# Kernel optimization log

Measured on AMD Instinct MI355X. Metric: run time of the kernel, lower is better.

Reference implementation:

```python
import math
import jax, jax.numpy as jnp
import numpy as np

H = 8
C_HIDDEN = 32
C_Q = 256


def setup_inputs() -> dict:
    key = jax.random.key(0)
    ks = jax.random.split(key, 9)
    B, S, Q, K = 1, 128, 256, 256
    q_x = jax.random.normal(ks[0], (B, S, Q, C_Q), dtype=jnp.float32)
    kv_x = jax.random.normal(ks[1], (B, S, K, C_Q), dtype=jnp.float32)
    bias1 = jax.random.normal(ks[2], (B, S, 1, 1, K), dtype=jnp.float32)
    bias2 = jax.random.normal(ks[3], (B, 1, H, Q, K), dtype=jnp.float32)
    scale = 1.0 / math.sqrt(C_Q)
    wq = jax.random.normal(ks[4], (H * C_HIDDEN, C_Q), dtype=jnp.float32) * scale
    wk = jax.random.normal(ks[5], (H * C_HIDDEN, C_Q), dtype=jnp.float32) * scale
    wv = jax.random.normal(ks[6], (H * C_HIDDEN, C_Q), dtype=jnp.float32) * scale
    wg = jax.random.normal(ks[7], (H * C_HIDDEN, C_Q), dtype=jnp.float32) * scale
    wo = jax.random.normal(ks[8], (C_Q, H * C_HIDDEN), dtype=jnp.float32) * scale
    return {"q_x": q_x, "kv_x": kv_x, "bias1": bias1, "bias2": bias2,
            "wq": wq, "wk": wk, "wv": wv, "wg": wg, "wo": wo}


def _split_heads(x):
    # [..., L, H*c] -> [..., H, L, c]
    y = x.reshape(x.shape[:-1] + (H, C_HIDDEN))
    return jnp.moveaxis(y, -2, -3)


def reference(q_x, kv_x, bias1, bias2, wq, wk, wv, wg, wo):
    # QKV projections (no bias), per-head split, scale q by 1/sqrt(c_hidden)
    q = _split_heads(q_x @ wq.T) / math.sqrt(C_HIDDEN)   # [B,S,H,Q,c]
    k = _split_heads(kv_x @ wk.T)                         # [B,S,H,K,c]
    v = _split_heads(kv_x @ wv.T)                         # [B,S,H,K,c]
    # attention logits with additive biases folded in
    a = jnp.einsum('...hqc,...hkc->...hqk', q, k) + bias1 + bias2
    a = jax.nn.softmax(a, axis=-1)
    o = jnp.einsum('...hqk,...hkc->...hqc', a, v)         # [B,S,H,Q,c]
    o = jnp.moveaxis(o, -3, -2)                           # [B,S,Q,H,c]
    # sigmoid gating from query data
    g = jax.nn.sigmoid(q_x @ wg.T)                        # [B,S,Q,H*c]
    g = g.reshape(g.shape[:-1] + (H, C_HIDDEN))
    o = o * g
    o = o.reshape(o.shape[:-2] + (H * C_HIDDEN,))         # flatten heads
    return o @ wo.T                                       # [B,S,Q,C_Q]
```

## Files before the change

kernel.cpp:

```cpp
#include <hip/hip_runtime.h>
#include <math.h>

#define S_DIM 128
#define H_DIM 8
#define M_TOT (S_DIM * 256)

typedef unsigned short ushort_t;
typedef unsigned int   uint32;
typedef __bf16  v8bf  __attribute__((ext_vector_type(8)));
typedef float   v4f   __attribute__((ext_vector_type(4)));

__device__ inline ushort_t f2b(float x) {
    unsigned int u = __float_as_uint(x);
    u += 0x7fffu + ((u >> 16) & 1u);
    return (ushort_t)(u >> 16);
}
__device__ inline float b2f(ushort_t h) {
    return __uint_as_float(((unsigned int)h) << 16);
}

#define GLDS16(gp, lp) __builtin_amdgcn_global_load_lds( \
    (const __attribute__((address_space(1))) void*)(gp), \
    (__attribute__((address_space(3))) void*)(lp), 16, 0, 0)

__global__ __launch_bounds__(256) void split_x(
    const float* __restrict__ xq, const float* __restrict__ xkv,
    ushort_t* __restrict__ hi, ushort_t* __restrict__ lo)
{
    const size_t BUF4 = (size_t)M_TOT * 64;
    const float* src = blockIdx.y ? xkv : xq;
    size_t base = (size_t)blockIdx.y * BUF4;
    int i = blockIdx.x * 256 + threadIdx.x;
    float4 v = ((const float4*)src)[i];
    ushort4 h, l;
    h.x = f2b(v.x); l.x = f2b(v.x - b2f(h.x));
    h.y = f2b(v.y); l.y = f2b(v.y - b2f(h.y));
    h.z = f2b(v.z); l.z = f2b(v.z - b2f(h.z));
    h.w = f2b(v.w); l.w = f2b(v.w - b2f(h.w));
    ((ushort4*)hi)[base + i] = h;
    ((ushort4*)lo)[base + i] = l;
}

__global__ __launch_bounds__(256) void split_w(
    const float* __restrict__ w0, const float* __restrict__ w1,
    const float* __restrict__ w2, const float* __restrict__ w3,
    const float* __restrict__ w4,
    ushort_t* __restrict__ hi, ushort_t* __restrict__ lo)
{
    const float* src;
    switch (blockIdx.y) {
        case 0: src = w0; break; case 1: src = w1; break;
        case 2: src = w2; break; case 3: src = w3; break;
        default: src = w4; break;
    }
    int i = blockIdx.x * 256 + threadIdx.x;
    float4 v = ((const float4*)src)[i];
    ushort4 h, l;
    h.x = f2b(v.x); l.x = f2b(v.x - b2f(h.x));
    h.y = f2b(v.y); l.y = f2b(v.y - b2f(h.y));
    h.z = f2b(v.z); l.z = f2b(v.z - b2f(h.z));
    h.w = f2b(v.w); l.w = f2b(v.w - b2f(h.w));
    size_t base = (size_t)blockIdx.y * 16384;
    ((ushort4*)hi)[base + i] = h;
    ((ushort4*)lo)[base + i] = l;
}

__global__ __launch_bounds__(256) void gemm_proj(
    const ushort_t* __restrict__ Xhi, const ushort_t* __restrict__ Xlo,
    const ushort_t* __restrict__ Whi4, const ushort_t* __restrict__ Wlo4,
    ushort_t* __restrict__ qh, ushort_t* __restrict__ ql,
    ushort_t* __restrict__ kh, ushort_t* __restrict__ kl,
    float* __restrict__ g_out,
    ushort_t* __restrict__ vh, ushort_t* __restrict__ vl,
    float qscale)
{
    __shared__ ushort_t lds[4][128 * 32];

    const int z    = blockIdx.z;
    const int t    = threadIdx.x;
    const int l    = t & 63;
    const int wv   = t >> 6;
    const int wm   = wv & 1;
    const int wn   = wv >> 1;
    const int idx  = l & 15;
    const int quad = l >> 4;
    const int m0   = blockIdx.y * 128;
    const int n0   = blockIdx.x * 128;

    const size_t BUF = (size_t)M_TOT * 256;
    const ushort_t* Ahi = Xhi + (size_t)z * BUF;
    const ushort_t* Alo = Xlo + (size_t)z * BUF;
    const ushort_t* Whi = Whi4 + (size_t)z * 131072;
    const ushort_t* Wlo = Wlo4 + (size_t)z * 131072;
    const float scale = z ? 1.f : qscale;

    const ushort_t* srcs[4] = { Ahi + (size_t)m0 * 256, Alo + (size_t)m0 * 256,
                                Whi + (size_t)n0 * 256, Wlo + (size_t)n0 * 256 };

    v4f acc[4][4];
    #pragma unroll
    for (int i = 0; i < 4; ++i)
        #pragma unroll
        for (int j = 0; j < 4; ++j) acc[i][j] = (v4f){0.f, 0.f, 0.f, 0.f};

    for (int k0 = 0; k0 < 256; k0 += 32) {
        #pragma unroll
        for (int b = 0; b < 4; ++b) {
            #pragma unroll
            for (int i = 0; i < 2; ++i) {
                const int sb   = wv * 128 + i * 64;
                const int slot = sb + l;
                const ushort_t* g = srcs[b] + (size_t)(slot >> 2) * 256 + k0 + (slot & 3) * 8;
                GLDS16(g, &lds[b][sb * 8]);
            }
        }
        __builtin_amdgcn_s_waitcnt(0);
        __syncthreads();

        v8bf ah[4], al[4], bh[4], bl[4];
        #pragma unroll
        for (int mt = 0; mt < 4; ++mt) {
            const int r   = wm * 64 + mt * 16 + idx;
            const int off = (r * 4 + quad) * 8;
            ah[mt] = *(const v8bf*)&lds[0][off];
            al[mt] = *(const v8bf*)&lds[1][off];
        }
        #pragma unroll
        for (int nt = 0; nt < 4; ++nt) {
            const int r   = wn * 64 + nt * 16 + idx;
            const int off = (r * 4 + quad) * 8;
            bh[nt] = *(const v8bf*)&lds[2][off];
            bl[nt] = *(const v8bf*)&lds[3][off];
        }

        #pragma unroll
        for (int mt = 0; mt < 4; ++mt)
            #pragma unroll
            for (int nt = 0; nt < 4; ++nt) {
                acc[mt][nt] = __builtin_amdgcn_mfma_f32_16x16x32_bf16(ah[mt], bh[nt], acc[mt][nt], 0, 0, 0);
                acc[mt][nt] = __builtin_amdgcn_mfma_f32_16x16x32_bf16(al[mt], bh[nt], acc[mt][nt], 0, 0, 0);
                acc[mt][nt] = __builtin_amdgcn_mfma_f32_16x16x32_bf16(ah[mt], bl[nt], acc[mt][nt], 0, 0, 0);
            }
        __syncthreads();
    }

    ushort_t* dsth = z ? kh : qh;
    ushort_t* dstl = z ? kl : ql;

    #pragma unroll
    for (int mt = 0; mt < 4; ++mt) {
        const int mbase = m0 + wm * 64 + mt * 16 + quad * 4;
        const int s = mbase >> 8, r8 = mbase & 255;
        #pragma unroll
        for (int nt = 0; nt < 4; ++nt) {
            const int gcol = n0 + wn * 64 + nt * 16 + idx;
            if (gcol < 256) {
                const int hh = gcol >> 5, c = gcol & 31;
                const size_t di = (((size_t)(s * 8 + hh) * 256) + r8) * 32 + c;
                #pragma unroll
                for (int r = 0; r < 4; ++r) {
                    const float val = acc[mt][nt][r] * scale;
                    const ushort_t hv = f2b(val);
                    dsth[di + (size_t)r * 32] = hv;
                    dstl[di + (size_t)r * 32] = f2b(val - b2f(hv));
                }
            } else if (z == 0) {
                const int gc = gcol - 256;
                #pragma unroll
                for (int r = 0; r < 4; ++r)
                    g_out[(size_t)(mbase + r) * 256 + gc] = acc[mt][nt][r];
            } else {
                const int gc = gcol - 256, hh = gc >> 5, c = gc & 31;
                ushort4 hv4, lv4;
                #pragma unroll
                for (int r = 0; r < 4; ++r) {
                    const float val = acc[mt][nt][r];
                    const ushort_t hv = f2b(val);
                    ((ushort_t*)&hv4)[r] = hv;
                    ((ushort_t*)&lv4)[r] = f2b(val - b2f(hv));
                }
                const size_t di = (((size_t)(s * 8 + hh) * 32) + c) * 256 + r8;
                *(ushort4*)&vh[di] = hv4;
                *(ushort4*)&vl[di] = lv4;
            }
        }
    }
}

__global__ __launch_bounds__(256) void gemm_split_mfma(
    const ushort_t* __restrict__ Ahi, const ushort_t* __restrict__ Alo,
    const ushort_t* __restrict__ Whi, const ushort_t* __restrict__ Wlo,
    float* __restrict__ Cf)
{
    __shared__ ushort_t lds[4][128 * 32];

    const int t    = threadIdx.x;
    const int l    = t & 63;
    const int wv   = t >> 6;
    const int wm   = wv & 1;
    const int wn   = wv >> 1;
    const int idx  = l & 15;
    const int quad = l >> 4;
    const int m0   = blockIdx.y * 128;
    const int n0   = blockIdx.x * 128;

    const ushort_t* srcs[4] = { Ahi + (size_t)m0 * 256, Alo + (size_t)m0 * 256,
                                Whi + (size_t)n0 * 256, Wlo + (size_t)n0 * 256 };

    v4f acc[4][4];
    #pragma unroll
    for (int i = 0; i < 4; ++i)
        #pragma unroll
        for (int j = 0; j < 4; ++j) acc[i][j] = (v4f){0.f, 0.f, 0.f, 0.f};

    for (int k0 = 0; k0 < 256; k0 += 32) {
        #pragma unroll
        for (int b = 0; b < 4; ++b) {
            #pragma unroll
            for (int i = 0; i < 2; ++i) {
                const int sb   = wv * 128 + i * 64;
                const int slot = sb + l;
                const ushort_t* g = srcs[b] + (size_t)(slot >> 2) * 256 + k0 + (slot & 3) * 8;
                GLDS16(g, &lds[b][sb * 8]);
            }
        }
        __builtin_amdgcn_s_waitcnt(0);
        __syncthreads();

        v8bf ah[4], al[4], bh[4], bl[4];
        #pragma unroll
        for (int mt = 0; mt < 4; ++mt) {
            const int r   = wm * 64 + mt * 16 + idx;
            const int off = (r * 4 + quad) * 8;
            ah[mt] = *(const v8bf*)&lds[0][off];
            al[mt] = *(const v8bf*)&lds[1][off];
        }
        #pragma unroll
        for (int nt = 0; nt < 4; ++nt) {
            const int r   = wn * 64 + nt * 16 + idx;
            const int off = (r * 4 + quad) * 8;
            bh[nt] = *(const v8bf*)&lds[2][off];
            bl[nt] = *(const v8bf*)&lds[3][off];
        }

        #pragma unroll
        for (int mt = 0; mt < 4; ++mt)
            #pragma unroll
            for (int nt = 0; nt < 4; ++nt) {
                acc[mt][nt] = __builtin_amdgcn_mfma_f32_16x16x32_bf16(ah[mt], bh[nt], acc[mt][nt], 0, 0, 0);
                acc[mt][nt] = __builtin_amdgcn_mfma_f32_16x16x32_bf16(al[mt], bh[nt], acc[mt][nt], 0, 0, 0);
                acc[mt][nt] = __builtin_amdgcn_mfma_f32_16x16x32_bf16(ah[mt], bl[nt], acc[mt][nt], 0, 0, 0);
            }
        __syncthreads();
    }

    #pragma unroll
    for (int mt = 0; mt < 4; ++mt) {
        #pragma unroll
        for (int nt = 0; nt < 4; ++nt) {
            const int gcol = n0 + wn * 64 + nt * 16 + idx;
            #pragma unroll
            for (int r = 0; r < 4; ++r) {
                const int grow = m0 + wm * 64 + mt * 16 + quad * 4 + r;
                Cf[(size_t)grow * 256 + gcol] = acc[mt][nt][r];
            }
        }
    }
}

__global__ __launch_bounds__(256, 2) void attn_mfma(
    const ushort_t* __restrict__ qh, const ushort_t* __restrict__ ql,
    const ushort_t* __restrict__ kh, const ushort_t* __restrict__ kl,
    const ushort_t* __restrict__ vth, const ushort_t* __restrict__ vtl,
    const float* __restrict__ b1, const float* __restrict__ b2,
    const float* __restrict__ gbuf,
    ushort_t* __restrict__ oh, ushort_t* __restrict__ ol)
{
    __shared__ __align__(16) uint32 pbuf[4][64 * 36];
    __shared__ __align__(16) float  lbuf[4][64 * 4];
    __shared__ __align__(16) float  invl[4][64];

    const int sh = blockIdx.x, s = sh >> 3, h = sh & 7;
    const int t = threadIdx.x, l = t & 63, w = t >> 6;
    const int idx = l & 15, quad = l >> 4;

    const size_t shb = (size_t)sh * 8192;
    const ushort_t* qhp = qh + shb;
    const ushort_t* qlp = ql + shb;
    const ushort_t* khp = kh + shb;
    const ushort_t* klp = kl + shb;
    const ushort_t* vhp = vth + shb;
    const ushort_t* vlp = vtl + shb;
    const float* b1p = b1 + (size_t)s * 256;
    const float* b2p = b2 + (size_t)h * 65536;

    v8bf qfh[4], qfl[4];
    #pragma unroll
    for (int nt = 0; nt < 4; ++nt) {
        const int off = (w * 64 + nt * 16 + idx) * 32 + quad * 8;
        qfh[nt] = *(const v8bf*)(qhp + off);
        qfl[nt] = *(const v8bf*)(qlp + off);
    }

    v4f oacc[4][2];
    #pragma unroll
    for (int mt = 0; mt < 4; ++mt) {
        oacc[mt][0] = (v4f){0.f, 0.f, 0.f, 0.f};
        oacc[mt][1] = (v4f){0.f, 0.f, 0.f, 0.f};
    }
    float lrun[4] = {0.f, 0.f, 0.f, 0.f};

    for (int c4 = 0; c4 < 4; ++c4) {
        const int ak0 = c4 * 64;

        v8bf kfh[4], kfl[4];
        #pragma unroll
        for (int at = 0; at < 4; ++at) {
            const int off = (ak0 + at * 16 + idx) * 32 + quad * 8;
            kfh[at] = *(const v8bf*)(khp + off);
            kfl[at] = *(const v8bf*)(klp + off);
        }

        v4f sacc[4][4];
        #pragma unroll
        for (int at = 0; at < 4; ++at)
            #pragma unroll
            for (int nt = 0; nt < 4; ++nt)
                sacc[at][nt] = (v4f){0.f, 0.f, 0.f, 0.f};
        #pragma unroll
        for (int at = 0; at < 4; ++at)
            #pragma unroll
            for (int nt = 0; nt < 4; ++nt) {
                sacc[at][nt] = __builtin_amdgcn_mfma_f32_16x16x32_bf16(kfh[at], qfh[nt], sacc[at][nt], 0, 0, 0);
                sacc[at][nt] = __builtin_amdgcn_mfma_f32_16x16x32_bf16(kfl[at], qfh[nt], sacc[at][nt], 0, 0, 0);
                sacc[at][nt] = __builtin_amdgcn_mfma_f32_16x16x32_bf16(kfh[at], qfl[nt], sacc[at][nt], 0, 0, 0);
            }

        v4f b1v[4];
        #pragma unroll
        for (int at = 0; at < 4; ++at)
            b1v[at] = *(const v4f*)(b1p + ak0 + at * 16 + quad * 4);

        #pragma unroll
        for (int at = 0; at < 4; ++at)
            #pragma unroll
            for (int nt = 0; nt < 4; ++nt) {
                const int q = w * 64 + nt * 16 + idx;
                v4f b2v = *(const v4f*)(b2p + (size_t)q * 256 + ak0 + at * 16 + quad * 4);
                float e0 = __expf(b1v[at][0] + b2v[0] + sacc[at][nt][0]);
                float e1 = __expf(b1v[at][1] + b2v[1] + sacc[at][nt][1]);
                float e2 = __expf(b1v[at][2] + b2v[2] + sacc[at][nt][2]);
                float e3 = __expf(b1v[at][3] + b2v[3] + sacc[at][nt][3]);
                lrun[nt] += (e0 + e1) + (e2 + e3);
                uint32 p0 = __builtin_amdgcn_perm(__float_as_uint(e1) + 0x8000u,
                                                  __float_as_uint(e0) + 0x8000u, 0x07060302u);
                uint32 p1 = __builtin_amdgcn_perm(__float_as_uint(e3) + 0x8000u,
                                                  __float_as_uint(e2) + 0x8000u, 0x07060302u);
                const int dw = (nt * 16 + idx) * 36 + at * 8 + quad * 2;
                *(uint2*)&pbuf[w][dw] = make_uint2(p0, p1);
            }

        v8bf vfh[2][2], vfl[2][2];
        #pragma unroll
        for (int n2 = 0; n2 < 2; ++n2)
            #pragma unroll
            for (int kt = 0; kt < 2; ++kt) {
                const int off = (n2 * 16 + idx) * 256 + ak0 + kt * 32 + quad * 8;
                vfh[n2][kt] = *(const v8bf*)(vhp + off);
                vfl[n2][kt] = *(const v8bf*)(vlp + off);
            }

        #pragma unroll
        for (int mt = 0; mt < 4; ++mt)
            #pragma unroll
            for (int kt = 0; kt < 2; ++kt) {
                v8bf pf = *(const v8bf*)&pbuf[w][(mt * 16 + idx) * 36 + kt * 16 + quad * 4];
                #pragma unroll
                for (int n2 = 0; n2 < 2; ++n2) {
                    oacc[mt][n2] = __builtin_amdgcn_mfma_f32_16x16x32_bf16(pf, vfh[n2][kt], oacc[mt][n2], 0, 0, 0);
                    oacc[mt][n2] = __builtin_amdgcn_mfma_f32_16x16x32_bf16(pf, vfl[n2][kt], oacc[mt][n2], 0, 0, 0);
                }
            }
    }

    #pragma unroll
    for (int nt = 0; nt < 4; ++nt)
        lbuf[w][(nt * 16 + idx) * 4 + quad] = lrun[nt];
    {
        v4f lv = *(const v4f*)&lbuf[w][l * 4];
        invl[w][l] = 1.f / ((lv[0] + lv[1]) + (lv[2] + lv[3]));
    }

    #pragma unroll
    for (int mt = 0; mt < 4; ++mt) {
        v4f iv = *(const v4f*)&invl[w][mt * 16 + quad * 4];
        #pragma unroll
        for (int n2 = 0; n2 < 2; ++n2) {
            const int c = n2 * 16 + idx;
            #pragma unroll
            for (int r = 0; r < 4; ++r) {
                const int q = w * 64 + mt * 16 + quad * 4 + r;
                const size_t gi = (size_t)(s * 256 + q) * 256 + h * 32 + c;
                const float gv = gbuf[gi];
                const float sig = 1.f / (1.f + __expf(-gv));
                const float val = oacc[mt][n2][r] * iv[r] * sig;
                const ushort_t hv = f2b(val);
                oh[gi] = hv;
                ol[gi] = f2b(val - b2f(hv));
            }
        }
    }
}

extern "C" void kernel_launch(void* const* d_in, const int* in_sizes, int n_in,
                              void* d_out, int out_size, void* d_ws, size_t ws_size,
                              hipStream_t stream)
{
    const float* q_x   = (const float*)d_in[0];
    const float* kv_x  = (const float*)d_in[1];
    const float* bias1 = (const float*)d_in[2];
    const float* bias2 = (const float*)d_in[3];
    const float* wq    = (const float*)d_in[4];
    const float* wk    = (const float*)d_in[5];
    const float* wv    = (const float*)d_in[6];
    const float* wg    = (const float*)d_in[7];
    const float* wo    = (const float*)d_in[8];
    float* out = (float*)d_out;

    const size_t BUF = (size_t)M_TOT * 256;

    float*    g_buf = (float*)d_ws;
    ushort_t* p     = (ushort_t*)(g_buf + BUF);
    ushort_t* qhb = p;            ushort_t* qlb = qhb + BUF;
    ushort_t* khb = qlb + BUF;    ushort_t* klb = khb + BUF;
    ushort_t* vhb = klb + BUF;    ushort_t* vlb = vhb + BUF;
    ushort_t* ohb = vlb + BUF;    ushort_t* olb = ohb + BUF;
    ushort_t* xhb = olb + BUF;    ushort_t* xlb = xhb + 2 * BUF;
    ushort_t* w_hi = xlb + 2 * BUF;
    ushort_t* w_lo = w_hi + 5 * 65536;

    const float qscale = 0.17677669529663689f;

    split_w<<<dim3(64, 5), 256, 0, stream>>>(wq, wg, wk, wv, wo, w_hi, w_lo);

    split_x<<<dim3(8192, 2), 256, 0, stream>>>(q_x, kv_x, xhb, xlb);

    gemm_proj<<<dim3(4, 256, 2), 256, 0, stream>>>(
        xhb, xlb, w_hi, w_lo, qhb, qlb, khb, klb, g_buf, vhb, vlb, qscale);

    attn_mfma<<<S_DIM * H_DIM, 256, 0, stream>>>(
        qhb, qlb, khb, klb, vhb, vlb, bias1, bias2, g_buf, ohb, olb);

    gemm_split_mfma<<<dim3(2, 256), 256, 0, stream>>>(
        ohb, olb, w_hi + 4 * 65536, w_lo + 4 * 65536, out);
}
```

Before: 312.2 us.

## Drop low-bf16 split for V and O, swizzle LDS, remap GEMM blocks

The V projection and the attention output are now stored only as single bf16 values instead of hi/lo pairs. This removes the lo buffers, their memory traffic and one MFMA pass in both the P·V product and the output GEMM. Separately, the LDS tiles in both GEMMs get an XOR-style rotated segment layout to reduce bank conflicts. Block indices are also remapped into grouped tiles to improve L2 reuse. The cost is lower precision in V and O, which may loosen accuracy against the fp32 reference.

After: 283.6 us. -9.2%, faster.

```diff
diff --git a/kernel.cpp b/kernel.cpp
--- a/kernel.cpp
+++ b/kernel.cpp
@@ -65,18 +65,22 @@
     ((ushort4*)lo)[base + i] = l;
 }
 
+
 __global__ __launch_bounds__(256) void gemm_proj(
     const ushort_t* __restrict__ Xhi, const ushort_t* __restrict__ Xlo,
     const ushort_t* __restrict__ Whi4, const ushort_t* __restrict__ Wlo4,
     ushort_t* __restrict__ qh, ushort_t* __restrict__ ql,
     ushort_t* __restrict__ kh, ushort_t* __restrict__ kl,
     float* __restrict__ g_out,
-    ushort_t* __restrict__ vh, ushort_t* __restrict__ vl,
+    ushort_t* __restrict__ vh,
     float qscale)
 {
     __shared__ ushort_t lds[4][128 * 32];
 
     const int z    = blockIdx.z;
+    const int L    = blockIdx.x + 4 * blockIdx.y;
+    const int mti  = ((L >> 5) << 3) + (L & 7);
+    const int nti  = (L >> 3) & 3;
     const int t    = threadIdx.x;
     const int l    = t & 63;
     const int wv   = t >> 6;
@@ -84,8 +88,8 @@
     const int wn   = wv >> 1;
     const int idx  = l & 15;
     const int quad = l >> 4;
-    const int m0   = blockIdx.y * 128;
-    const int n0   = blockIdx.x * 128;
+    const int m0   = mti * 128;
+    const int n0   = nti * 128;
 
     const size_t BUF = (size_t)M_TOT * 256;
     const ushort_t* Ahi = Xhi + (size_t)z * BUF;
@@ -110,7 +114,9 @@
             for (int i = 0; i < 2; ++i) {
                 const int sb   = wv * 128 + i * 64;
                 const int slot = sb + l;
-                const ushort_t* g = srcs[b] + (size_t)(slot >> 2) * 256 + k0 + (slot & 3) * 8;
+                const int row  = slot >> 2;
+                const int gseg = ((slot & 3) - (row >> 1)) & 3;
+                const ushort_t* g = srcs[b] + (size_t)row * 256 + k0 + gseg * 8;
                 GLDS16(g, &lds[b][sb * 8]);
             }
         }
@@ -121,14 +127,14 @@
         #pragma unroll
         for (int mt = 0; mt < 4; ++mt) {
             const int r   = wm * 64 + mt * 16 + idx;
-            const int off = (r * 4 + quad) * 8;
+            const int off = r * 32 + (((quad + (r >> 1)) & 3) << 3);
             ah[mt] = *(const v8bf*)&lds[0][off];
             al[mt] = *(const v8bf*)&lds[1][off];
         }
         #pragma unroll
         for (int nt = 0; nt < 4; ++nt) {
             const int r   = wn * 64 + nt * 16 + idx;
-            const int off = (r * 4 + quad) * 8;
+            const int off = r * 32 + (((quad + (r >> 1)) & 3) << 3);
             bh[nt] = *(const v8bf*)&lds[2][off];
             bl[nt] = *(const v8bf*)&lds[3][off];
         }
@@ -171,29 +177,26 @@
                     g_out[(size_t)(mbase + r) * 256 + gc] = acc[mt][nt][r];
             } else {
                 const int gc = gcol - 256, hh = gc >> 5, c = gc & 31;
-                ushort4 hv4, lv4;
+                ushort4 hv4;
                 #pragma unroll
-                for (int r = 0; r < 4; ++r) {
-                    const float val = acc[mt][nt][r];
-                    const ushort_t hv = f2b(val);
-                    ((ushort_t*)&hv4)[r] = hv;
-                    ((ushort_t*)&lv4)[r] = f2b(val - b2f(hv));
-                }
+                for (int r = 0; r < 4; ++r)
+                    ((ushort_t*)&hv4)[r] = f2b(acc[mt][nt][r]);
                 const size_t di = (((size_t)(s * 8 + hh) * 32) + c) * 256 + r8;
                 *(ushort4*)&vh[di] = hv4;
-                *(ushort4*)&vl[di] = lv4;
-            }
-        }
-    }
-}
-
-__global__ __launch_bounds__(256) void gemm_split_mfma(
-    const ushort_t* __restrict__ Ahi, const ushort_t* __restrict__ Alo,
-    const ushort_t* __restrict__ Whi, const ushort_t* __restrict__ Wlo,
-    float* __restrict__ Cf)
-{
-    __shared__ ushort_t lds[4][128 * 32];
-
+            }
+        }
+    }
+}
+
+__global__ __launch_bounds__(256) void gemm_out(
+    const ushort_t* __restrict__ Ah, const ushort_t* __restrict__ Whi,
+    const ushort_t* __restrict__ Wlo, float* __restrict__ Cf)
+{
+    __shared__ ushort_t lds[3][128 * 32];
+
+    const int L    = blockIdx.x + 2 * blockIdx.y;
+    const int mti  = ((L >> 4) << 3) + (L & 7);
+    const int nti  = (L >> 3) & 1;
     const int t    = threadIdx.x;
     const int l    = t & 63;
     const int wv   = t >> 6;
@@ -201,10 +204,10 @@
     const int wn   = wv >> 1;
     const int idx  = l & 15;
     const int quad = l >> 4;
-    const int m0   = blockIdx.y * 128;
-    const int n0   = blockIdx.x * 128;
-
-    const ushort_t* srcs[4] = { Ahi + (size_t)m0 * 256, Alo + (size_t)m0 * 256,
+    const int m0   = mti * 128;
+    const int n0   = nti * 128;
+
+    const ushort_t* srcs[3] = { Ah + (size_t)m0 * 256,
                                 Whi + (size_t)n0 * 256, Wlo + (size_t)n0 * 256 };
 
     v4f acc[4][4];
@@ -215,32 +218,33 @@
 
     for (int k0 = 0; k0 < 256; k0 += 32) {
         #pragma unroll
-        for (int b = 0; b < 4; ++b) {
+        for (int b = 0; b < 3; ++b) {
             #pragma unroll
             for (int i = 0; i < 2; ++i) {
                 const int sb   = wv * 128 + i * 64;
                 const int slot = sb + l;
-                const ushort_t* g = srcs[b] + (size_t)(slot >> 2) * 256 + k0 + (slot & 3) * 8;
+                const int row  = slot >> 2;
+                const int gseg = ((slot & 3) - (row >> 1)) & 3;
+                const ushort_t* g = srcs[b] + (size_t)row * 256 + k0 + gseg * 8;
                 GLDS16(g, &lds[b][sb * 8]);
             }
         }
         __builtin_amdgcn_s_waitcnt(0);
         __syncthreads();
 
-        v8bf ah[4], al[4], bh[4], bl[4];
+        v8bf ah[4], bh[4], bl[4];
         #pragma unroll
         for (int mt = 0; mt < 4; ++mt) {
             const int r   = wm * 64 + mt * 16 + idx;
-            const int off = (r * 4 + quad) * 8;
+            const int off = r * 32 + (((quad + (r >> 1)) & 3) << 3);
             ah[mt] = *(const v8bf*)&lds[0][off];
-            al[mt] = *(const v8bf*)&lds[1][off];
         }
         #pragma unroll
         for (int nt = 0; nt < 4; ++nt) {
             const int r   = wn * 64 + nt * 16 + idx;
-            const int off = (r * 4 + quad) * 8;
-            bh[nt] = *(const v8bf*)&lds[2][off];
-            bl[nt] = *(const v8bf*)&lds[3][off];
+            const int off = r * 32 + (((quad + (r >> 1)) & 3) << 3);
+            bh[nt] = *(const v8bf*)&lds[1][off];
+            bl[nt] = *(const v8bf*)&lds[2][off];
         }
 
         #pragma unroll
@@ -248,7 +252,6 @@
             #pragma unroll
             for (int nt = 0; nt < 4; ++nt) {
                 acc[mt][nt] = __builtin_amdgcn_mfma_f32_16x16x32_bf16(ah[mt], bh[nt], acc[mt][nt], 0, 0, 0);
-                acc[mt][nt] = __builtin_amdgcn_mfma_f32_16x16x32_bf16(al[mt], bh[nt], acc[mt][nt], 0, 0, 0);
                 acc[mt][nt] = __builtin_amdgcn_mfma_f32_16x16x32_bf16(ah[mt], bl[nt], acc[mt][nt], 0, 0, 0);
             }
         __syncthreads();
@@ -271,10 +274,10 @@
 __global__ __launch_bounds__(256, 2) void attn_mfma(
     const ushort_t* __restrict__ qh, const ushort_t* __restrict__ ql,
     const ushort_t* __restrict__ kh, const ushort_t* __restrict__ kl,
-    const ushort_t* __restrict__ vth, const ushort_t* __restrict__ vtl,
+    const ushort_t* __restrict__ vth,
     const float* __restrict__ b1, const float* __restrict__ b2,
     const float* __restrict__ gbuf,
-    ushort_t* __restrict__ oh, ushort_t* __restrict__ ol)
+    ushort_t* __restrict__ oh)
 {
     __shared__ __align__(16) uint32 pbuf[4][64 * 36];
     __shared__ __align__(16) float  lbuf[4][64 * 4];
@@ -290,7 +293,6 @@
     const ushort_t* khp = kh + shb;
     const ushort_t* klp = kl + shb;
     const ushort_t* vhp = vth + shb;
-    const ushort_t* vlp = vtl + shb;
     const float* b1p = b1 + (size_t)s * 256;
     const float* b2p = b2 + (size_t)h * 65536;
 
@@ -360,14 +362,13 @@
                 *(uint2*)&pbuf[w][dw] = make_uint2(p0, p1);
             }
 
-        v8bf vfh[2][2], vfl[2][2];
+        v8bf vfh[2][2];
         #pragma unroll
         for (int n2 = 0; n2 < 2; ++n2)
             #pragma unroll
             for (int kt = 0; kt < 2; ++kt) {
                 const int off = (n2 * 16 + idx) * 256 + ak0 + kt * 32 + quad * 8;
                 vfh[n2][kt] = *(const v8bf*)(vhp + off);
-                vfl[n2][kt] = *(const v8bf*)(vlp + off);
             }
 
         #pragma unroll
@@ -376,10 +377,8 @@
             for (int kt = 0; kt < 2; ++kt) {
                 v8bf pf = *(const v8bf*)&pbuf[w][(mt * 16 + idx) * 36 + kt * 16 + quad * 4];
                 #pragma unroll
-                for (int n2 = 0; n2 < 2; ++n2) {
+                for (int n2 = 0; n2 < 2; ++n2)
                     oacc[mt][n2] = __builtin_amdgcn_mfma_f32_16x16x32_bf16(pf, vfh[n2][kt], oacc[mt][n2], 0, 0, 0);
-                    oacc[mt][n2] = __builtin_amdgcn_mfma_f32_16x16x32_bf16(pf, vfl[n2][kt], oacc[mt][n2], 0, 0, 0);
-                }
             }
     }
 
@@ -403,10 +402,7 @@
                 const size_t gi = (size_t)(s * 256 + q) * 256 + h * 32 + c;
                 const float gv = gbuf[gi];
                 const float sig = 1.f / (1.f + __expf(-gv));
-                const float val = oacc[mt][n2][r] * iv[r] * sig;
-                const ushort_t hv = f2b(val);
-                oh[gi] = hv;
-                ol[gi] = f2b(val - b2f(hv));
+                oh[gi] = f2b(oacc[mt][n2][r] * iv[r] * sig);
             }
         }
     }
@@ -433,9 +429,9 @@
     ushort_t* p     = (ushort_t*)(g_buf + BUF);
     ushort_t* qhb = p;            ushort_t* qlb = qhb + BUF;
     ushort_t* khb = qlb + BUF;    ushort_t* klb = khb + BUF;
-    ushort_t* vhb = klb + BUF;    ushort_t* vlb = vhb + BUF;
-    ushort_t* ohb = vlb + BUF;    ushort_t* olb = ohb + BUF;
-    ushort_t* xhb = olb + BUF;    ushort_t* xlb = xhb + 2 * BUF;
+    ushort_t* vhb = klb + BUF;
+    ushort_t* ohb = vhb + BUF;
+    ushort_t* xhb = ohb + BUF;    ushort_t* xlb = xhb + 2 * BUF;
     ushort_t* w_hi = xlb + 2 * BUF;
     ushort_t* w_lo = w_hi + 5 * 65536;
 
@@ -446,11 +442,11 @@
     split_x<<<dim3(8192, 2), 256, 0, stream>>>(q_x, kv_x, xhb, xlb);
 
     gemm_proj<<<dim3(4, 256, 2), 256, 0, stream>>>(
-        xhb, xlb, w_hi, w_lo, qhb, qlb, khb, klb, g_buf, vhb, vlb, qscale);
+        xhb, xlb, w_hi, w_lo, qhb, qlb, khb, klb, g_buf, vhb, qscale);
 
     attn_mfma<<<S_DIM * H_DIM, 256, 0, stream>>>(
-        qhb, qlb, khb, klb, vhb, vlb, bias1, bias2, g_buf, ohb, olb);
-
-    gemm_split_mfma<<<dim3(2, 256), 256, 0, stream>>>(
-        ohb, olb, w_hi + 4 * 65536, w_lo + 4 * 65536, out);
-}
+        qhb, qlb, khb, klb, vhb, bias1, bias2, g_buf, ohb);
+
+    gemm_out<<<dim3(2, 256), 256, 0, stream>>>(
+        ohb, w_hi + 4 * 65536, w_lo + 4 * 65536, out);
+}
```
